# Kernel optimization log

Hardware: AMD Instinct MI355X
Metric: run time of the kernel (lower is better)

The kernel has to match this reference:

```python
import jax, jax.numpy as jnp
import numpy as np

NUM_HEADS = 16
HEAD_DIM = 64
D_MODEL = 1024
WINDOW = 256
ROPE_BASE = 10000.0
LN_EPS = 1e-5


def setup_inputs() -> dict:
    key = jax.random.key(0)
    k1, k2, k3, k4 = jax.random.split(key, 4)
    B, S, D = 1, 2048, D_MODEL
    x = jax.random.normal(k1, (B, S, D), dtype=jnp.float32)
    state = jax.random.normal(k2, (B, D), dtype=jnp.float32)
    # nn.Linear(d, 3d, bias=False): y = x @ W_qkv with W_qkv: [D, 3D]
    W_qkv = jax.random.normal(k3, (D, 3 * D), dtype=jnp.float32) / np.sqrt(D)
    W_out = jax.random.normal(k4, (D, D), dtype=jnp.float32) / np.sqrt(D)
    ln_gamma = jnp.ones((D,), dtype=jnp.float32)
    ln_beta = jnp.zeros((D,), dtype=jnp.float32)
    return {"x": x, "state": state, "W_qkv": W_qkv, "W_out": W_out,
            "ln_gamma": ln_gamma, "ln_beta": ln_beta}


def _rotate_half(t):
    h = t.shape[-1] // 2
    return jnp.concatenate([-t[..., h:], t[..., :h]], axis=-1)


def _rope(q, k):
    # q, k: [B, H, S, Hd]
    S, Hd = q.shape[2], q.shape[3]
    inv_freq = 1.0 / (ROPE_BASE ** (jnp.arange(0, Hd, 2, dtype=jnp.float32) / Hd))
    ang = jnp.arange(S, dtype=jnp.float32)[:, None] * inv_freq[None, :]  # [S, Hd/2]
    cos = jnp.concatenate([jnp.cos(ang), jnp.cos(ang)], axis=-1)[None, None]  # [1,1,S,Hd]
    sin = jnp.concatenate([jnp.sin(ang), jnp.sin(ang)], axis=-1)[None, None]
    return q * cos + _rotate_half(q) * sin, k * cos + _rotate_half(k) * sin


def _local_causal_mask(S):
    idx = jnp.arange(S)
    dist = idx[:, None] - idx[None, :]
    allowed = (dist >= 0) & (dist <= WINDOW)
    # Faithful to source: allowed positions get 1.0 (softmax-shift-invariant), else -inf
    return jnp.where(allowed, 1.0, -jnp.inf).astype(jnp.float32)[None, None]


def reference(x, state, W_qkv, W_out, ln_gamma, ln_beta):
    B, S, D = x.shape
    H, Hd = NUM_HEADS, HEAD_DIM
    qkv = (x @ W_qkv).reshape(B, S, 3, H, Hd).transpose(2, 0, 3, 1, 4)  # [3,B,H,S,Hd]
    q, k, v = qkv[0], qkv[1], qkv[2]
    q, k = _rope(q, k)
    scores = jnp.einsum("bhsd,bhtd->bhst", q, k) / np.sqrt(Hd) + _local_causal_mask(S)
    attn = jax.nn.softmax(scores, axis=-1)
    out = jnp.einsum("bhst,bhtd->bhsd", attn, v)  # [B,H,S,Hd]
    out = out.transpose(0, 2, 1, 3).reshape(B, S, D)
    res = x + out @ W_out
    mu = jnp.mean(res, axis=-1, keepdims=True)
    var = jnp.var(res, axis=-1, keepdims=True)
    y = (res - mu) * jax.lax.rsqrt(var + LN_EPS) * ln_gamma + ln_beta
    return y, state
```

## Files before the change

kernel.cpp:

```cpp
#include <hip/hip_runtime.h>
#include <math.h>

#define S_LEN 2048
#define DMODEL 1024
#define NHEADS 16
#define HDIM 64
#define WIN 256
#define N_QKV 3072

typedef __attribute__((ext_vector_type(8))) short s16x8;
typedef __attribute__((ext_vector_type(8))) _Float16 f16x8;
typedef __attribute__((ext_vector_type(4))) _Float16 f16x4;
typedef __attribute__((ext_vector_type(4))) float f32x4;

__device__ inline unsigned short f2bf(float f) {
    unsigned int u = __float_as_uint(f);
    u += 0x7FFFu + ((u >> 16) & 1u);
    return (unsigned short)(u >> 16);
}
__device__ inline float bf2f(unsigned short h) {
    return __uint_as_float(((unsigned int)h) << 16);
}

__global__ __launch_bounds__(256) void cvt_f16(
    const float* __restrict__ src, _Float16* __restrict__ dst)
{
    int i = blockIdx.x * 256 + threadIdx.x;
    float4 v = *(const float4*)&src[i * 4];
    f16x4 o;
    o[0] = (_Float16)v.x; o[1] = (_Float16)v.y;
    o[2] = (_Float16)v.z; o[3] = (_Float16)v.w;
    *(f16x4*)&dst[i * 4] = o;
}

__global__ __launch_bounds__(256) void transpose_cvt(
    const float* __restrict__ W, _Float16* __restrict__ T, int K, int N)
{
    __shared__ float t[32][33];
    const int tx = threadIdx.x & 31;
    const int ty = threadIdx.x >> 5;
    const int n0 = blockIdx.x * 32, k0 = blockIdx.y * 32;

    #pragma unroll
    for (int i = 0; i < 4; ++i)
        t[ty + i * 8][tx] = W[(size_t)(k0 + ty + i * 8) * N + n0 + tx];
    __syncthreads();
    #pragma unroll
    for (int i = 0; i < 4; ++i) {
        int n = n0 + ty + i * 8;
        T[(size_t)n * K + k0 + tx] = (_Float16)t[tx][ty + i * 8];
    }
}

template<int BM, int BN, int WM, int WN, bool RES>
__global__ __launch_bounds__(256) void gemm_f16(
    const _Float16* __restrict__ A, const _Float16* __restrict__ B,
    const float* __restrict__ resid, float* __restrict__ C,
    int M, int N, int K)
{
    constexpr int MI = WM / 16;
    constexpr int NJ = WN / 16;
    constexpr int APASS = BM / 64;
    constexpr int BPASS = BN / 64;
    static_assert(WM * 2 == BM && WN * 2 == BN, "4 waves as 2x2");

    __shared__ _Float16 As[BM * 32];
    __shared__ _Float16 Bs[BN * 32];

    const int tid  = threadIdx.x;
    const int w    = tid >> 6;
    const int lane = tid & 63;
    const int m16  = lane & 15;
    const int g    = lane >> 4;
    const int wr   = w >> 1, wc = w & 1;
    const int bm   = blockIdx.y * BM, bn = blockIdx.x * BN;

    f32x4 acc[MI][NJ];
    #pragma unroll
    for (int i = 0; i < MI; ++i)
        #pragma unroll
        for (int j = 0; j < NJ; ++j) acc[i][j] = (f32x4)(0.0f);

    uint4 ra[APASS], rb[BPASS];

    #pragma unroll
    for (int p = 0; p < APASS; ++p) {
        int f = p * 256 + tid, row = f >> 2, cb = f & 3;
        ra[p] = *(const uint4*)&A[(size_t)(bm + row) * K + cb * 8];
    }
    #pragma unroll
    for (int p = 0; p < BPASS; ++p) {
        int f = p * 256 + tid, row = f >> 2, cb = f & 3;
        rb[p] = *(const uint4*)&B[(size_t)(bn + row) * K + cb * 8];
    }

    const int NT = K / 32;
    for (int kt = 0; kt < NT; ++kt) {
        __syncthreads();
        #pragma unroll
        for (int p = 0; p < APASS; ++p) {
            int f = p * 256 + tid, row = f >> 2, cb = f & 3;
            *(uint4*)&As[row * 32 + ((cb ^ ((row >> 1) & 3)) << 3)] = ra[p];
        }
        #pragma unroll
        for (int p = 0; p < BPASS; ++p) {
            int f = p * 256 + tid, row = f >> 2, cb = f & 3;
            *(uint4*)&Bs[row * 32 + ((cb ^ ((row >> 1) & 3)) << 3)] = rb[p];
        }
        __syncthreads();

        if (kt + 1 < NT) {
            int k0 = (kt + 1) * 32;
            #pragma unroll
            for (int p = 0; p < APASS; ++p) {
                int f = p * 256 + tid, row = f >> 2, cb = f & 3;
                ra[p] = *(const uint4*)&A[(size_t)(bm + row) * K + k0 + cb * 8];
            }
            #pragma unroll
            for (int p = 0; p < BPASS; ++p) {
                int f = p * 256 + tid, row = f >> 2, cb = f & 3;
                rb[p] = *(const uint4*)&B[(size_t)(bn + row) * K + k0 + cb * 8];
            }
        }

        f16x8 af[MI], bf_[NJ];
        #pragma unroll
        for (int i = 0; i < MI; ++i) {
            int row = wr * WM + i * 16 + m16;
            af[i] = *(const f16x8*)&As[row * 32 + ((g ^ ((row >> 1) & 3)) << 3)];
        }
        #pragma unroll
        for (int j = 0; j < NJ; ++j) {
            int row = wc * WN + j * 16 + m16;
            bf_[j] = *(const f16x8*)&Bs[row * 32 + ((g ^ ((row >> 1) & 3)) << 3)];
        }
        #pragma unroll
        for (int j = 0; j < NJ; ++j)
            #pragma unroll
            for (int i = 0; i < MI; ++i)
                acc[i][j] = __builtin_amdgcn_mfma_f32_16x16x32_f16(
                    af[i], bf_[j], acc[i][j], 0, 0, 0);
    }

    const int g4 = g * 4;
    #pragma unroll
    for (int i = 0; i < MI; ++i)
        #pragma unroll
        for (int j = 0; j < NJ; ++j) {
            int col = bn + wc * WN + j * 16 + m16;
            #pragma unroll
            for (int r = 0; r < 4; ++r) {
                int row = bm + wr * WM + i * 16 + g4 + r;
                float val = acc[i][j][r];
                if (RES) val += resid[(size_t)row * N + col];
                C[(size_t)row * N + col] = val;
            }
        }
}

__global__ __launch_bounds__(256) void rope_scatter(
    const float* __restrict__ qkv, float* __restrict__ q,
    unsigned short* __restrict__ khi, unsigned short* __restrict__ klo)
{
    int idx = blockIdx.x * 256 + threadIdx.x;
    int s  = idx >> 10;
    int r  = idx & 1023;
    int hd = r & 63;
    int h  = r >> 6;
    const float* row = qkv + (size_t)s * N_QKV;

    float qv = row[r];
    float kv = row[DMODEL + r];

    int   i   = hd & 31;
    float inv = expf(-(float)i * 0.2878231366242553f);
    float ang = (float)s * inv;
    float c  = cosf(ang);
    float sn = sinf(ang);

    int   pr  = (hd < 32) ? r + 32 : r - 32;
    float sgn = (hd < 32) ? -1.0f : 1.0f;

    float qo = qv * c + sgn * row[pr] * sn;
    float ko = kv * c + sgn * row[DMODEL + pr] * sn;

    size_t o = ((size_t)h * S_LEN + s) * HDIM + hd;
    q[o] = qo;
    unsigned short kh = f2bf(ko);
    khi[o] = kh;
    klo[o] = f2bf(ko - bf2f(kh));
}

__global__ __launch_bounds__(256) void v_transpose(
    const float* __restrict__ qkv, unsigned short* __restrict__ vT)
{
    __shared__ float t[64][65];
    const int s0 = blockIdx.x * 64;
    const int h  = blockIdx.y;
    const int tid = threadIdx.x;
    const int dq  = (tid & 15) * 4;
    const int sl0 = tid >> 4;

    #pragma unroll
    for (int p = 0; p < 4; ++p) {
        int sl = sl0 + p * 16;
        float4 v = *(const float4*)&qkv[(size_t)(s0 + sl) * N_QKV + 2 * DMODEL + h * HDIM + dq];
        t[sl][dq] = v.x; t[sl][dq + 1] = v.y; t[sl][dq + 2] = v.z; t[sl][dq + 3] = v.w;
    }
    __syncthreads();
    #pragma unroll
    for (int p = 0; p < 2; ++p) {
        int u = tid + p * 256;
        int d = u >> 3, sb = (u & 7) * 8;
        s16x8 o;
        #pragma unroll
        for (int i = 0; i < 8; ++i) o[i] = (short)f2bf(t[sb + i][d]);
        *(s16x8*)&vT[((size_t)h * HDIM + d) * S_LEN + s0 + sb] = o;
    }
}

#define KP 72
__global__ __launch_bounds__(256, 3) void attn_mfma(
    const float* __restrict__ qg, const unsigned short* __restrict__ khg,
    const unsigned short* __restrict__ klg, const unsigned short* __restrict__ vTg,
    _Float16* __restrict__ oh)
{
    __shared__ __align__(16) unsigned short Kh[64][KP], Kl[64][KP], Vt[64][KP];
    __shared__ __align__(16) unsigned short Pw[4][16][40];

    const int h   = blockIdx.y;
    const int s0  = blockIdx.x * 64;
    const int tid = threadIdx.x;
    const int w   = tid >> 6, lane = tid & 63;
    const int m16 = lane & 15, g = lane >> 4;
    const int t_base = s0 - 256;

    const int qrow = s0 + w * 16 + m16;
    const float* qp = qg + ((size_t)h * S_LEN + qrow) * HDIM;
    s16x8 qh[2], ql[2];
    #pragma unroll
    for (int c = 0; c < 2; ++c) {
        float4 f0 = *(const float4*)&qp[c * 32 + g * 8];
        float4 f1 = *(const float4*)&qp[c * 32 + g * 8 + 4];
        float f[8] = {f0.x, f0.y, f0.z, f0.w, f1.x, f1.y, f1.z, f1.w};
        #pragma unroll
        for (int j = 0; j < 8; ++j) {
            float v = f[j] * 0.125f;
            unsigned short hb = f2bf(v);
            qh[c][j] = (short)hb;
            ql[c][j] = (short)f2bf(v - bf2f(hb));
        }
    }

    const int qb = w * 16 + m16;
    int lo_b = 256 - s0; if (lo_b < qb) lo_b = qb;
    const int hi_b = qb + 256;

    f32x4 O[4];
    #pragma unroll
    for (int nt = 0; nt < 4; ++nt) O[nt] = (f32x4)(0.0f);
    float l_r[4] = {0.0f, 0.0f, 0.0f, 0.0f};
    float m_col = -1e30f;

    const int stage_min = (s0 >= 256) ? 0 : ((193 - s0 + 63) >> 6);

    for (int st = stage_min; st < 5; ++st) {
        __syncthreads();
        const int t0s = t_base + st * 64;
        #pragma unroll
        for (int pp = 0; pp < 2; ++pp) {
            int u = tid + pp * 256;
            int row = u >> 3, cb = (u & 7) * 8;
            int t = t0s + row;
            s16x8 vh = {}, vl = {};
            if (t >= 0) {
                size_t base = ((size_t)h * S_LEN + t) * HDIM + cb;
                vh = *(const s16x8*)&khg[base];
                vl = *(const s16x8*)&klg[base];
            }
            *(s16x8*)&Kh[row][cb] = vh;
            *(s16x8*)&Kl[row][cb] = vl;
        }
        #pragma unroll
        for (int pp = 0; pp < 2; ++pp) {
            int u = tid + pp * 256;
            int d = u >> 3, kb = (u & 7) * 8;
            int t = t0s + kb;
            s16x8 vv = {};
            if (t >= 0)
                vv = *(const s16x8*)&vTg[((size_t)h * HDIM + d) * S_LEN + t];
            *(s16x8*)&Vt[d][kb] = vv;
        }
        __syncthreads();

        #pragma unroll
        for (int ch = 0; ch < 2; ++ch) {
            f32x4 sc[2];
            #pragma unroll
            for (int kt2 = 0; kt2 < 2; ++kt2) {
                int krow = ch * 32 + kt2 * 16 + m16;
                s16x8 kh0 = *(const s16x8*)&Kh[krow][g * 8];
                s16x8 kh1 = *(const s16x8*)&Kh[krow][32 + g * 8];
                s16x8 kl0 = *(const s16x8*)&Kl[krow][g * 8];
                s16x8 kl1 = *(const s16x8*)&Kl[krow][32 + g * 8];
                f32x4 a = (f32x4)(0.0f);
                a = __builtin_amdgcn_mfma_f32_16x16x32_bf16(kh0, qh[0], a, 0, 0, 0);
                a = __builtin_amdgcn_mfma_f32_16x16x32_bf16(kh1, qh[1], a, 0, 0, 0);
                a = __builtin_amdgcn_mfma_f32_16x16x32_bf16(kh0, ql[0], a, 0, 0, 0);
                a = __builtin_amdgcn_mfma_f32_16x16x32_bf16(kh1, ql[1], a, 0, 0, 0);
                a = __builtin_amdgcn_mfma_f32_16x16x32_bf16(kl0, qh[0], a, 0, 0, 0);
                a = __builtin_amdgcn_mfma_f32_16x16x32_bf16(kl1, qh[1], a, 0, 0, 0);
                sc[kt2] = a;
            }

            float scm[8];
            float pmax = -1e30f;
            #pragma unroll
            for (int kt2 = 0; kt2 < 2; ++kt2)
                #pragma unroll
                for (int r = 0; r < 4; ++r) {
                    int ki = st * 64 + ch * 32 + kt2 * 16 + 4 * g + r;
                    bool vd = (ki >= lo_b) && (ki <= hi_b);
                    float s_ = vd ? sc[kt2][r] : -1e30f;
                    scm[kt2 * 4 + r] = s_;
                    pmax = fmaxf(pmax, s_);
                }
            pmax = fmaxf(pmax, __shfl_xor(pmax, 16));
            pmax = fmaxf(pmax, __shfl_xor(pmax, 32));
            float mnew = fmaxf(m_col, pmax);

            float p[8];
            float psum = 0.0f;
            #pragma unroll
            for (int i = 0; i < 8; ++i) {
                float e = (scm[i] > -9e29f) ? __expf(scm[i] - mnew) : 0.0f;
                p[i] = e;
                psum += e;
            }
            psum += __shfl_xor(psum, 16);
            psum += __shfl_xor(psum, 32);
            float scale = __expf(m_col - mnew);
            m_col = mnew;

            #pragma unroll
            for (int r = 0; r < 4; ++r) {
                float sr = __shfl(scale, 4 * g + r);
                float ps = __shfl(psum, 4 * g + r);
                l_r[r] = l_r[r] * sr + ps;
                O[0][r] *= sr; O[1][r] *= sr; O[2][r] *= sr; O[3][r] *= sr;
            }

            unsigned int d0, d1, d2, d3;
            asm("v_cvt_pk_bf16_f32 %0, %1, %2" : "=v"(d0) : "v"(p[0]), "v"(p[1]));
            asm("v_cvt_pk_bf16_f32 %0, %1, %2" : "=v"(d1) : "v"(p[2]), "v"(p[3]));
            asm("v_cvt_pk_bf16_f32 %0, %1, %2" : "=v"(d2) : "v"(p[4]), "v"(p[5]));
            asm("v_cvt_pk_bf16_f32 %0, %1, %2" : "=v"(d3) : "v"(p[6]), "v"(p[7]));
            *(uint2*)&Pw[w][m16][4 * g]      = make_uint2(d0, d1);
            *(uint2*)&Pw[w][m16][16 + 4 * g] = make_uint2(d2, d3);
            asm volatile("s_waitcnt lgkmcnt(0)" ::: "memory");
            __builtin_amdgcn_sched_barrier(0);
            s16x8 pa = *(const s16x8*)&Pw[w][m16][g * 8];

            #pragma unroll
            for (int nt = 0; nt < 4; ++nt) {
                s16x8 vb = *(const s16x8*)&Vt[nt * 16 + m16][ch * 32 + g * 8];
                O[nt] = __builtin_amdgcn_mfma_f32_16x16x32_bf16(pa, vb, O[nt], 0, 0, 0);
            }
        }
    }

    #pragma unroll
    for (int r = 0; r < 4; ++r) {
        float linv = 1.0f / l_r[r];
        int srow = s0 + w * 16 + 4 * g + r;
        size_t obase = (size_t)srow * DMODEL + h * HDIM;
        #pragma unroll
        for (int nt = 0; nt < 4; ++nt)
            oh[obase + nt * 16 + m16] = (_Float16)(O[nt][r] * linv);
    }
}

__global__ __launch_bounds__(256) void layernorm_k(
    const float* __restrict__ res, const float* __restrict__ gamma,
    const float* __restrict__ beta, float* __restrict__ y)
{
    const int row  = blockIdx.x;
    const int tid  = threadIdx.x;
    const int wave = tid >> 6;
    const int lane = tid & 63;
    const float* r = res + (size_t)row * DMODEL;

    float4 xv = *(const float4*)&r[tid * 4];
    float ssum = xv.x + xv.y + xv.z + xv.w;
    float ssq  = xv.x * xv.x + xv.y * xv.y + xv.z * xv.z + xv.w * xv.w;

    #pragma unroll
    for (int off = 1; off < 64; off <<= 1) {
        ssum += __shfl_xor(ssum, off);
        ssq  += __shfl_xor(ssq, off);
    }

    __shared__ float wsum[4], wsq[4];
    if (lane == 0) { wsum[wave] = ssum; wsq[wave] = ssq; }
    __syncthreads();

    float tot  = wsum[0] + wsum[1] + wsum[2] + wsum[3];
    float tot2 = wsq[0] + wsq[1] + wsq[2] + wsq[3];
    float mu   = tot * (1.0f / DMODEL);
    float var  = tot2 * (1.0f / DMODEL) - mu * mu;
    float rstd = rsqrtf(var + 1e-5f);

    float4 gm = *(const float4*)&gamma[tid * 4];
    float4 be = *(const float4*)&beta[tid * 4];
    float4 yo;
    yo.x = (xv.x - mu) * rstd * gm.x + be.x;
    yo.y = (xv.y - mu) * rstd * gm.y + be.y;
    yo.z = (xv.z - mu) * rstd * gm.z + be.z;
    yo.w = (xv.w - mu) * rstd * gm.w + be.w;
    *(float4*)&y[(size_t)row * DMODEL + tid * 4] = yo;
}

extern "C" void kernel_launch(void* const* d_in, const int* in_sizes, int n_in,
                              void* d_out, int out_size, void* d_ws, size_t ws_size,
                              hipStream_t stream) {
    const float* x     = (const float*)d_in[0];
    const float* state = (const float*)d_in[1];
    const float* Wqkv  = (const float*)d_in[2];
    const float* Wout  = (const float*)d_in[3];
    const float* gamma = (const float*)d_in[4];
    const float* beta  = (const float*)d_in[5];
    float* out = (float*)d_out;

    char* base = (char*)d_ws;
    float*     qkv_raw = (float*)base;
    _Float16*  ah      = (_Float16*)base;
    float*     res     = (float*)(base + 8388608);
    float*          qb  = (float*)(base + 25165824);
    unsigned short* khi = (unsigned short*)(base + 33554432);
    unsigned short* klo = (unsigned short*)(base + 37748736);
    unsigned short* vT  = (unsigned short*)(base + 41943040);
    _Float16* WqkvT = (_Float16*)(base + 46137344);
    _Float16* WoutT = (_Float16*)(base + 52428800);
    _Float16* xh    = (_Float16*)(base + 54525952);

    cvt_f16<<<(S_LEN * DMODEL) / 1024, 256, 0, stream>>>(x, xh);
    transpose_cvt<<<dim3(N_QKV / 32, DMODEL / 32), 256, 0, stream>>>(
        Wqkv, WqkvT, DMODEL, N_QKV);
    transpose_cvt<<<dim3(DMODEL / 32, DMODEL / 32), 256, 0, stream>>>(
        Wout, WoutT, DMODEL, DMODEL);

    gemm_f16<128, 64, 64, 32, false>
        <<<dim3(N_QKV / 64, S_LEN / 128), 256, 0, stream>>>(
            xh, WqkvT, nullptr, qkv_raw, S_LEN, N_QKV, DMODEL);

    rope_scatter<<<(S_LEN * DMODEL) / 256, 256, 0, stream>>>(qkv_raw, qb, khi, klo);

    v_transpose<<<dim3(S_LEN / 64, NHEADS), 256, 0, stream>>>(qkv_raw, vT);

    attn_mfma<<<dim3(S_LEN / 64, NHEADS), 256, 0, stream>>>(
        qb, khi, klo, vT, ah);

    gemm_f16<64, 64, 32, 32, true>
        <<<dim3(DMODEL / 64, S_LEN / 64), 256, 0, stream>>>(
            ah, WoutT, x, res, S_LEN, DMODEL, DMODEL);

    layernorm_k<<<S_LEN, 256, 0, stream>>>(res, gamma, beta, out);

    hipMemcpyAsync(out + (size_t)S_LEN * DMODEL, state,
                   (size_t)DMODEL * sizeof(float),
                   hipMemcpyDeviceToDevice, stream);
}
```

Baseline: 185.1 us.

## Fuse RoPE and K/V scatter into QKV GEMM epilogue with larger tiles

The QKV GEMM now uses 128x128 tiles with a K-step of 64, and its epilogue applies RoPE from a precomputed cos/sin table. It writes Q as fp32, K as hi/lo bf16 splits and V as bf16 straight from registers, which removes the fp32 qkv intermediate and the separate rope_scatter pass. v_transpose now reads bf16 V, and the output GEMM moves to 128x64 tiles with K-step 64. The trade-offs are higher register and LDS use per block, fewer blocks in the first GEMM, and scattered epilogue stores.

```diff
diff --git a/kernel.cpp b/kernel.cpp
--- a/kernel.cpp
+++ b/kernel.cpp
@@ -33,6 +33,15 @@
     *(f16x4*)&dst[i * 4] = o;
 }
 
+__global__ __launch_bounds__(256) void rope_tab_k(float2* __restrict__ tab)
+{
+    int idx = blockIdx.x * 256 + threadIdx.x;
+    int s = idx >> 5, i = idx & 31;
+    float inv = expf(-(float)i * 0.2878231366242553f);
+    float ang = (float)s * inv;
+    tab[idx] = make_float2(cosf(ang), sinf(ang));
+}
+
 __global__ __launch_bounds__(256) void transpose_cvt(
     const float* __restrict__ W, _Float16* __restrict__ T, int K, int N)
 {
@@ -52,149 +61,223 @@
     }
 }
 
-template<int BM, int BN, int WM, int WN, bool RES>
-__global__ __launch_bounds__(256) void gemm_f16(
+__global__ __launch_bounds__(256) void gemm1_fused(
     const _Float16* __restrict__ A, const _Float16* __restrict__ B,
-    const float* __restrict__ resid, float* __restrict__ C,
-    int M, int N, int K)
-{
-    constexpr int MI = WM / 16;
-    constexpr int NJ = WN / 16;
-    constexpr int APASS = BM / 64;
-    constexpr int BPASS = BN / 64;
-    static_assert(WM * 2 == BM && WN * 2 == BN, "4 waves as 2x2");
-
-    __shared__ _Float16 As[BM * 32];
-    __shared__ _Float16 Bs[BN * 32];
-
-    const int tid  = threadIdx.x;
-    const int w    = tid >> 6;
-    const int lane = tid & 63;
-    const int m16  = lane & 15;
-    const int g    = lane >> 4;
-    const int wr   = w >> 1, wc = w & 1;
-    const int bm   = blockIdx.y * BM, bn = blockIdx.x * BN;
-
-    f32x4 acc[MI][NJ];
-    #pragma unroll
-    for (int i = 0; i < MI; ++i)
-        #pragma unroll
-        for (int j = 0; j < NJ; ++j) acc[i][j] = (f32x4)(0.0f);
-
-    uint4 ra[APASS], rb[BPASS];
-
-    #pragma unroll
-    for (int p = 0; p < APASS; ++p) {
-        int f = p * 256 + tid, row = f >> 2, cb = f & 3;
-        ra[p] = *(const uint4*)&A[(size_t)(bm + row) * K + cb * 8];
-    }
-    #pragma unroll
-    for (int p = 0; p < BPASS; ++p) {
-        int f = p * 256 + tid, row = f >> 2, cb = f & 3;
-        rb[p] = *(const uint4*)&B[(size_t)(bn + row) * K + cb * 8];
-    }
-
-    const int NT = K / 32;
-    for (int kt = 0; kt < NT; ++kt) {
+    const float2* __restrict__ tab,
+    float* __restrict__ qb, unsigned short* __restrict__ khb,
+    unsigned short* __restrict__ klb, unsigned short* __restrict__ vbf)
+{
+    constexpr int K = DMODEL;
+    __shared__ _Float16 As[128 * 64];
+    __shared__ _Float16 Bs[128 * 64];
+
+    const int tid = threadIdx.x;
+    const int w = tid >> 6, lane = tid & 63;
+    const int m16 = lane & 15, g = lane >> 4;
+    const int wr = w >> 1, wc = w & 1;
+    const int bm = blockIdx.y * 128, bn = blockIdx.x * 128;
+
+    f32x4 acc[4][4];
+    #pragma unroll
+    for (int i = 0; i < 4; ++i)
+        #pragma unroll
+        for (int j = 0; j < 4; ++j) acc[i][j] = (f32x4)(0.0f);
+
+    uint4 ra[4], rb[4];
+    #pragma unroll
+    for (int p = 0; p < 4; ++p) {
+        int f = p * 256 + tid, row = f >> 3, gr = f & 7;
+        ra[p] = *(const uint4*)&A[(size_t)(bm + row) * K + gr * 8];
+        rb[p] = *(const uint4*)&B[(size_t)(bn + row) * K + gr * 8];
+    }
+
+    for (int kt = 0; kt < 16; ++kt) {
         __syncthreads();
         #pragma unroll
-        for (int p = 0; p < APASS; ++p) {
-            int f = p * 256 + tid, row = f >> 2, cb = f & 3;
-            *(uint4*)&As[row * 32 + ((cb ^ ((row >> 1) & 3)) << 3)] = ra[p];
-        }
-        #pragma unroll
-        for (int p = 0; p < BPASS; ++p) {
-            int f = p * 256 + tid, row = f >> 2, cb = f & 3;
-            *(uint4*)&Bs[row * 32 + ((cb ^ ((row >> 1) & 3)) << 3)] = rb[p];
+        for (int p = 0; p < 4; ++p) {
+            int f = p * 256 + tid, row = f >> 3, gr = f & 7;
+            int slot = (gr ^ (row & 7)) << 3;
+            *(uint4*)&As[row * 64 + slot] = ra[p];
+            *(uint4*)&Bs[row * 64 + slot] = rb[p];
         }
         __syncthreads();
 
-        if (kt + 1 < NT) {
-            int k0 = (kt + 1) * 32;
-            #pragma unroll
-            for (int p = 0; p < APASS; ++p) {
-                int f = p * 256 + tid, row = f >> 2, cb = f & 3;
-                ra[p] = *(const uint4*)&A[(size_t)(bm + row) * K + k0 + cb * 8];
-            }
-            #pragma unroll
-            for (int p = 0; p < BPASS; ++p) {
-                int f = p * 256 + tid, row = f >> 2, cb = f & 3;
-                rb[p] = *(const uint4*)&B[(size_t)(bn + row) * K + k0 + cb * 8];
-            }
-        }
-
-        f16x8 af[MI], bf_[NJ];
-        #pragma unroll
-        for (int i = 0; i < MI; ++i) {
-            int row = wr * WM + i * 16 + m16;
-            af[i] = *(const f16x8*)&As[row * 32 + ((g ^ ((row >> 1) & 3)) << 3)];
-        }
-        #pragma unroll
-        for (int j = 0; j < NJ; ++j) {
-            int row = wc * WN + j * 16 + m16;
-            bf_[j] = *(const f16x8*)&Bs[row * 32 + ((g ^ ((row >> 1) & 3)) << 3)];
-        }
-        #pragma unroll
-        for (int j = 0; j < NJ; ++j)
-            #pragma unroll
-            for (int i = 0; i < MI; ++i)
-                acc[i][j] = __builtin_amdgcn_mfma_f32_16x16x32_f16(
-                    af[i], bf_[j], acc[i][j], 0, 0, 0);
+        if (kt < 15) {
+            int k0 = (kt + 1) * 64;
+            #pragma unroll
+            for (int p = 0; p < 4; ++p) {
+                int f = p * 256 + tid, row = f >> 3, gr = f & 7;
+                ra[p] = *(const uint4*)&A[(size_t)(bm + row) * K + k0 + gr * 8];
+                rb[p] = *(const uint4*)&B[(size_t)(bn + row) * K + k0 + gr * 8];
+            }
+        }
+
+        #pragma unroll
+        for (int kh = 0; kh < 2; ++kh) {
+            f16x8 af[4], bf_[4];
+            #pragma unroll
+            for (int i = 0; i < 4; ++i) {
+                int row = wr * 64 + i * 16 + m16;
+                af[i] = *(const f16x8*)&As[row * 64 + (((kh * 4 + g) ^ (row & 7)) << 3)];
+            }
+            #pragma unroll
+            for (int j = 0; j < 4; ++j) {
+                int row = wc * 64 + j * 16 + m16;
+                bf_[j] = *(const f16x8*)&Bs[row * 64 + (((kh * 4 + g) ^ (row & 7)) << 3)];
+            }
+            #pragma unroll
+            for (int j = 0; j < 4; ++j)
+                #pragma unroll
+                for (int i = 0; i < 4; ++i)
+                    acc[i][j] = __builtin_amdgcn_mfma_f32_16x16x32_f16(
+                        af[i], bf_[j], acc[i][j], 0, 0, 0);
+        }
+    }
+
+    const int u = blockIdx.x * 2 + wc;
+    const int sbase = bm + wr * 64;
+    if (u < 32) {
+        const int h = (u < 16) ? u : u - 16;
+        #pragma unroll
+        for (int j = 0; j < 2; ++j) {
+            const int hd_lo = j * 16 + m16;
+            #pragma unroll
+            for (int i = 0; i < 4; ++i)
+                #pragma unroll
+                for (int r = 0; r < 4; ++r) {
+                    int s = sbase + i * 16 + 4 * g + r;
+                    float2 cs = tab[s * 32 + hd_lo];
+                    float vlo = acc[i][j][r], vhi = acc[i][j + 2][r];
+                    float rlo = vlo * cs.x - vhi * cs.y;
+                    float rhi = vhi * cs.x + vlo * cs.y;
+                    size_t o = ((size_t)h * S_LEN + s) * HDIM + hd_lo;
+                    if (u < 16) {
+                        qb[o] = rlo;
+                        qb[o + 32] = rhi;
+                    } else {
+                        unsigned short hb = f2bf(rlo);
+                        khb[o] = hb; klb[o] = f2bf(rlo - bf2f(hb));
+                        hb = f2bf(rhi);
+                        khb[o + 32] = hb; klb[o + 32] = f2bf(rhi - bf2f(hb));
+                    }
+                }
+        }
+    } else {
+        const int hv = u - 32;
+        #pragma unroll
+        for (int j = 0; j < 4; ++j)
+            #pragma unroll
+            for (int i = 0; i < 4; ++i)
+                #pragma unroll
+                for (int r = 0; r < 4; ++r) {
+                    int s = sbase + i * 16 + 4 * g + r;
+                    vbf[(size_t)s * DMODEL + hv * HDIM + j * 16 + m16] =
+                        f2bf(acc[i][j][r]);
+                }
+    }
+}
+
+__global__ __launch_bounds__(256) void gemm2_k(
+    const _Float16* __restrict__ A, const _Float16* __restrict__ B,
+    const float* __restrict__ resid, float* __restrict__ C)
+{
+    constexpr int K = DMODEL;
+    __shared__ _Float16 As[128 * 64];
+    __shared__ _Float16 Bs[64 * 64];
+
+    const int tid = threadIdx.x;
+    const int w = tid >> 6, lane = tid & 63;
+    const int m16 = lane & 15, g = lane >> 4;
+    const int wr = w >> 1, wc = w & 1;
+    const int bm = blockIdx.y * 128, bn = blockIdx.x * 64;
+
+    f32x4 acc[4][2];
+    #pragma unroll
+    for (int i = 0; i < 4; ++i)
+        #pragma unroll
+        for (int j = 0; j < 2; ++j) acc[i][j] = (f32x4)(0.0f);
+
+    uint4 ra[4], rb[2];
+    #pragma unroll
+    for (int p = 0; p < 4; ++p) {
+        int f = p * 256 + tid, row = f >> 3, gr = f & 7;
+        ra[p] = *(const uint4*)&A[(size_t)(bm + row) * K + gr * 8];
+    }
+    #pragma unroll
+    for (int p = 0; p < 2; ++p) {
+        int f = p * 256 + tid, row = f >> 3, gr = f & 7;
+        rb[p] = *(const uint4*)&B[(size_t)(bn + row) * K + gr * 8];
+    }
+
+    for (int kt = 0; kt < 16; ++kt) {
+        __syncthreads();
+        #pragma unroll
+        for (int p = 0; p < 4; ++p) {
+            int f = p * 256 + tid, row = f >> 3, gr = f & 7;
+            *(uint4*)&As[row * 64 + ((gr ^ (row & 7)) << 3)] = ra[p];
+        }
+        #pragma unroll
+        for (int p = 0; p < 2; ++p) {
+            int f = p * 256 + tid, row = f >> 3, gr = f & 7;
+            *(uint4*)&Bs[row * 64 + ((gr ^ (row & 7)) << 3)] = rb[p];
+        }
+        __syncthreads();
+
+        if (kt < 15) {
+            int k0 = (kt + 1) * 64;
+            #pragma unroll
+            for (int p = 0; p < 4; ++p) {
+                int f = p * 256 + tid, row = f >> 3, gr = f & 7;
+                ra[p] = *(const uint4*)&A[(size_t)(bm + row) * K + k0 + gr * 8];
+            }
+            #pragma unroll
+            for (int p = 0; p < 2; ++p) {
+                int f = p * 256 + tid, row = f >> 3, gr = f & 7;
+                rb[p] = *(const uint4*)&B[(size_t)(bn + row) * K + k0 + gr * 8];
+            }
+        }
+
+        #pragma unroll
+        for (int kh = 0; kh < 2; ++kh) {
+            f16x8 af[4], bf_[2];
+            #pragma unroll
+            for (int i = 0; i < 4; ++i) {
+                int row = wr * 64 + i * 16 + m16;
+                af[i] = *(const f16x8*)&As[row * 64 + (((kh * 4 + g) ^ (row & 7)) << 3)];
+            }
+            #pragma unroll
+            for (int j = 0; j < 2; ++j) {
+                int row = wc * 32 + j * 16 + m16;
+                bf_[j] = *(const f16x8*)&Bs[row * 64 + (((kh * 4 + g) ^ (row & 7)) << 3)];
+            }
+            #pragma unroll
+            for (int j = 0; j < 2; ++j)
+                #pragma unroll
+                for (int i = 0; i < 4; ++i)
+                    acc[i][j] = __builtin_amdgcn_mfma_f32_16x16x32_f16(
+                        af[i], bf_[j], acc[i][j], 0, 0, 0);
+        }
     }
 
     const int g4 = g * 4;
     #pragma unroll
-    for (int i = 0; i < MI; ++i)
-        #pragma unroll
-        for (int j = 0; j < NJ; ++j) {
-            int col = bn + wc * WN + j * 16 + m16;
+    for (int i = 0; i < 4; ++i)
+        #pragma unroll
+        for (int j = 0; j < 2; ++j) {
+            int col = bn + wc * 32 + j * 16 + m16;
             #pragma unroll
             for (int r = 0; r < 4; ++r) {
-                int row = bm + wr * WM + i * 16 + g4 + r;
-                float val = acc[i][j][r];
-                if (RES) val += resid[(size_t)row * N + col];
-                C[(size_t)row * N + col] = val;
-            }
-        }
-}
-
-__global__ __launch_bounds__(256) void rope_scatter(
-    const float* __restrict__ qkv, float* __restrict__ q,
-    unsigned short* __restrict__ khi, unsigned short* __restrict__ klo)
-{
-    int idx = blockIdx.x * 256 + threadIdx.x;
-    int s  = idx >> 10;
-    int r  = idx & 1023;
-    int hd = r & 63;
-    int h  = r >> 6;
-    const float* row = qkv + (size_t)s * N_QKV;
-
-    float qv = row[r];
-    float kv = row[DMODEL + r];
-
-    int   i   = hd & 31;
-    float inv = expf(-(float)i * 0.2878231366242553f);
-    float ang = (float)s * inv;
-    float c  = cosf(ang);
-    float sn = sinf(ang);
-
-    int   pr  = (hd < 32) ? r + 32 : r - 32;
-    float sgn = (hd < 32) ? -1.0f : 1.0f;
-
-    float qo = qv * c + sgn * row[pr] * sn;
-    float ko = kv * c + sgn * row[DMODEL + pr] * sn;
-
-    size_t o = ((size_t)h * S_LEN + s) * HDIM + hd;
-    q[o] = qo;
-    unsigned short kh = f2bf(ko);
-    khi[o] = kh;
-    klo[o] = f2bf(ko - bf2f(kh));
+                int row = bm + wr * 64 + i * 16 + g4 + r;
+                C[(size_t)row * DMODEL + col] =
+                    acc[i][j][r] + resid[(size_t)row * DMODEL + col];
+            }
+        }
 }
 
 __global__ __launch_bounds__(256) void v_transpose(
-    const float* __restrict__ qkv, unsigned short* __restrict__ vT)
-{
-    __shared__ float t[64][65];
+    const unsigned short* __restrict__ vbf, unsigned short* __restrict__ vT)
+{
+    __shared__ unsigned short t[64][72];
     const int s0 = blockIdx.x * 64;
     const int h  = blockIdx.y;
     const int tid = threadIdx.x;
@@ -204,7 +287,7 @@
     #pragma unroll
     for (int p = 0; p < 4; ++p) {
         int sl = sl0 + p * 16;
-        float4 v = *(const float4*)&qkv[(size_t)(s0 + sl) * N_QKV + 2 * DMODEL + h * HDIM + dq];
+        ushort4 v = *(const ushort4*)&vbf[(size_t)(s0 + sl) * DMODEL + h * HDIM + dq];
         t[sl][dq] = v.x; t[sl][dq + 1] = v.y; t[sl][dq + 2] = v.z; t[sl][dq + 3] = v.w;
     }
     __syncthreads();
@@ -214,7 +297,7 @@
         int d = u >> 3, sb = (u & 7) * 8;
         s16x8 o;
         #pragma unroll
-        for (int i = 0; i < 8; ++i) o[i] = (short)f2bf(t[sb + i][d]);
+        for (int i = 0; i < 8; ++i) o[i] = (short)t[sb + i][d];
         *(s16x8*)&vT[((size_t)h * HDIM + d) * S_LEN + s0 + sb] = o;
     }
 }
@@ -252,9 +335,9 @@
         }
     }
 
-    const int qb = w * 16 + m16;
-    int lo_b = 256 - s0; if (lo_b < qb) lo_b = qb;
-    const int hi_b = qb + 256;
+    const int qb_ = w * 16 + m16;
+    int lo_b = 256 - s0; if (lo_b < qb_) lo_b = qb_;
+    const int hi_b = qb_ + 256;
 
     f32x4 O[4];
     #pragma unroll
@@ -432,37 +515,35 @@
     float* out = (float*)d_out;
 
     char* base = (char*)d_ws;
-    float*     qkv_raw = (float*)base;
-    _Float16*  ah      = (_Float16*)base;
-    float*     res     = (float*)(base + 8388608);
-    float*          qb  = (float*)(base + 25165824);
-    unsigned short* khi = (unsigned short*)(base + 33554432);
-    unsigned short* klo = (unsigned short*)(base + 37748736);
-    unsigned short* vT  = (unsigned short*)(base + 41943040);
-    _Float16* WqkvT = (_Float16*)(base + 46137344);
-    _Float16* WoutT = (_Float16*)(base + 52428800);
-    _Float16* xh    = (_Float16*)(base + 54525952);
+    _Float16*       ah    = (_Float16*)(base + 0);
+    float*          res   = (float*)(base + 4194304);
+    float*          qb    = (float*)(base + 12582912);
+    unsigned short* khb   = (unsigned short*)(base + 20971520);
+    unsigned short* klb   = (unsigned short*)(base + 25165824);
+    unsigned short* vbf   = (unsigned short*)(base + 29360128);
+    unsigned short* vT    = (unsigned short*)(base + 33554432);
+    _Float16*       WqkvT = (_Float16*)(base + 37748736);
+    _Float16*       WoutT = (_Float16*)(base + 44040192);
+    _Float16*       xh    = (_Float16*)(base + 46137344);
+    float2*         tab   = (float2*)(base + 50331648);
 
     cvt_f16<<<(S_LEN * DMODEL) / 1024, 256, 0, stream>>>(x, xh);
+    rope_tab_k<<<(S_LEN * 32) / 256, 256, 0, stream>>>(tab);
     transpose_cvt<<<dim3(N_QKV / 32, DMODEL / 32), 256, 0, stream>>>(
         Wqkv, WqkvT, DMODEL, N_QKV);
     transpose_cvt<<<dim3(DMODEL / 32, DMODEL / 32), 256, 0, stream>>>(
         Wout, WoutT, DMODEL, DMODEL);
 
-    gemm_f16<128, 64, 64, 32, false>
-        <<<dim3(N_QKV / 64, S_LEN / 128), 256, 0, stream>>>(
-            xh, WqkvT, nullptr, qkv_raw, S_LEN, N_QKV, DMODEL);
-
-    rope_scatter<<<(S_LEN * DMODEL) / 256, 256, 0, stream>>>(qkv_raw, qb, khi, klo);
-
-    v_transpose<<<dim3(S_LEN / 64, NHEADS), 256, 0, stream>>>(qkv_raw, vT);
+    gemm1_fused<<<dim3(N_QKV / 128, S_LEN / 128), 256, 0, stream>>>(
+        xh, WqkvT, tab, qb, khb, klb, vbf);
+
+    v_transpose<<<dim3(S_LEN / 64, NHEADS), 256, 0, stream>>>(vbf, vT);
 
     attn_mfma<<<dim3(S_LEN / 64, NHEADS), 256, 0, stream>>>(
-        qb, khi, klo, vT, ah);
-
-    gemm_f16<64, 64, 32, 32, true>
-        <<<dim3(DMODEL / 64, S_LEN / 64), 256, 0, stream>>>(
-            ah, WoutT, x, res, S_LEN, DMODEL, DMODEL);
+        qb, khb, klb, vT, ah);
+
+    gemm2_k<<<dim3(DMODEL / 64, S_LEN / 128), 256, 0, stream>>>(
+        ah, WoutT, x, res);
 
     layernorm_k<<<S_LEN, 256, 0, stream>>>(res, gamma, beta, out);
 
```

Result: slower. 253.2 us (+36.8%).
